# Performance work log

Measured on AMD Instinct MI355X. Metric: run time of the kernel, lower is better.

The kernel has to match this reference:

```python
import jax, jax.numpy as jnp
import numpy as np

NUM_EMBEDDINGS = 4096
EMBEDDING_DIM = 256


def setup_inputs() -> dict:
    key = jax.random.key(0)
    k1, k2 = jax.random.split(key)
    inputs = jax.random.normal(k1, (16, 4096, EMBEDDING_DIM), dtype=jnp.float32)
    embeddings = jax.random.normal(k2, (NUM_EMBEDDINGS, EMBEDDING_DIM), dtype=jnp.float32)
    return {"inputs": inputs, "embeddings": embeddings}


def reference(inputs, embeddings):
    input_shape = inputs.shape
    flat = inputs.reshape(-1, EMBEDDING_DIM)                     # [N, D]
    input_sq = jnp.sum(flat * flat, axis=1, keepdims=True)       # [N, 1]
    emb_sq = jnp.sum(embeddings * embeddings, axis=1)            # [K]
    distances = input_sq - 2.0 * (flat @ embeddings.T) + emb_sq  # [N, K]
    encoding_indices = jnp.argmin(distances, axis=1)             # [N]
    quantized = embeddings[encoding_indices].reshape(input_shape)
    encoding_indices = encoding_indices.reshape(input_shape[:-1])
    # use_commitment=False path: codebook loss only (quantized detached)
    loss = jnp.mean((jax.lax.stop_gradient(quantized) - inputs) ** 2)
    # straight-through estimator
    quantized_st = inputs + jax.lax.stop_gradient(quantized - inputs)
    return (quantized_st, loss, encoding_indices)
```

## Files before the change

### kernel.cpp

```cpp
#include <hip/hip_runtime.h>
#include <float.h>
#include <stdint.h>


#define DDIM 256
#define KCODES 4096
#define NROWS 65536
#define QSIZE 16777216
#define NSLOT 64
#define NLBLK 16384
#define GAP_THRESH 0.02f

#define O_FCOUNT 4097
#define O_FLAGS 4100
#define O_IDXF 69636
#define O_LPART 135172
#define O_EMBH 151556
#define O_EMBL 675844
#define O_AH 1200384
#define O_AL 9588992
#define WS_NEED_FLOATS 17977600ull

typedef short bf16x8 __attribute__((ext_vector_type(8)));
typedef float f32x4 __attribute__((ext_vector_type(4)));

__device__ __forceinline__ void gload_lds16(const void* g, void* l) {
    __builtin_amdgcn_global_load_lds(
        (const __attribute__((address_space(1))) void*)g,
        (__attribute__((address_space(3))) void*)l, 16, 0, 0);
}

__global__ __launch_bounds__(64) void esq_conv(const float* __restrict__ emb,
                                               float* __restrict__ ws,
                                               short* __restrict__ eh,
                                               short* __restrict__ el) {
    int c = blockIdx.x, l = threadIdx.x;
    const float4* e4 = (const float4*)(emb + (size_t)c * DDIM);
    float4 v = e4[l];
    float s = v.x * v.x + v.y * v.y + v.z * v.z + v.w * v.w;
    float f[4] = {v.x, v.y, v.z, v.w};
    uint32_t hu[4], lu[4];
#pragma unroll
    for (int k = 0; k < 4; ++k) {
        uint32_t u = __float_as_uint(f[k]);
        uint32_t h = u & 0xFFFF0000u;
        hu[k] = h;
        lu[k] = __float_as_uint(f[k] - __uint_as_float(h));
    }
    uint2 hv, lv;
    hv.x = __builtin_amdgcn_perm(hu[1], hu[0], 0x07060302u);
    hv.y = __builtin_amdgcn_perm(hu[3], hu[2], 0x07060302u);
    lv.x = __builtin_amdgcn_perm(lu[1], lu[0], 0x07060302u);
    lv.y = __builtin_amdgcn_perm(lu[3], lu[2], 0x07060302u);
    *(uint2*)&eh[(size_t)c * DDIM + l * 4] = hv;
    *(uint2*)&el[(size_t)c * DDIM + l * 4] = lv;
#pragma unroll
    for (int off = 32; off >= 1; off >>= 1) s += __shfl_down(s, off);
    if (l == 0) ws[c] = s;
    if (c == 0 && l == 0) ((int*)ws)[O_FCOUNT] = 0;
}

__device__ __forceinline__ void conv8(float4 a, float4 b,
                                      short* __restrict__ dh,
                                      short* __restrict__ dl) {
    float f[8] = {a.x, a.y, a.z, a.w, b.x, b.y, b.z, b.w};
    uint32_t hu[8], lu[8];
#pragma unroll
    for (int k = 0; k < 8; ++k) {
        uint32_t u = __float_as_uint(f[k]);
        uint32_t h = u & 0xFFFF0000u;
        hu[k] = h;
        lu[k] = __float_as_uint(f[k] - __uint_as_float(h));
    }
    uint4 hv, lv;
    hv.x = __builtin_amdgcn_perm(hu[1], hu[0], 0x07060302u);
    hv.y = __builtin_amdgcn_perm(hu[3], hu[2], 0x07060302u);
    hv.z = __builtin_amdgcn_perm(hu[5], hu[4], 0x07060302u);
    hv.w = __builtin_amdgcn_perm(hu[7], hu[6], 0x07060302u);
    lv.x = __builtin_amdgcn_perm(lu[1], lu[0], 0x07060302u);
    lv.y = __builtin_amdgcn_perm(lu[3], lu[2], 0x07060302u);
    lv.z = __builtin_amdgcn_perm(lu[5], lu[4], 0x07060302u);
    lv.w = __builtin_amdgcn_perm(lu[7], lu[6], 0x07060302u);
    *(uint4*)dh = hv;
    *(uint4*)dl = lv;
}

__device__ __forceinline__ void stage8(const float* __restrict__ p,
                                       short* __restrict__ dh,
                                       short* __restrict__ dl) {
    float4 a = *(const float4*)p;
    float4 b = *(const float4*)(p + 4);
    conv8(a, b, dh, dl);
}

__global__ __launch_bounds__(256) void inp_conv(const float* __restrict__ inp,
                                                short* __restrict__ ahg,
                                                short* __restrict__ alg) {
    size_t g = (size_t)blockIdx.x * 256 + threadIdx.x;
    const float* p = inp + g * 8;
    float4 a = *(const float4*)p;
    float4 b = *(const float4*)(p + 4);
    conv8(a, b, ahg + g * 8, alg + g * 8);
}

__global__ __launch_bounds__(512, 6) void vq_gemm(const short* __restrict__ ahg,
                                                  const short* __restrict__ alg,
                                                  const short* __restrict__ ehg,
                                                  const short* __restrict__ elg,
                                                  const float* __restrict__ esq,
                                                  float2* __restrict__ pmin2,
                                                  int* __restrict__ pidx) {
    __shared__ __align__(16) short Ah[128 * 32];
    __shared__ __align__(16) short Al[128 * 32];
    __shared__ __align__(16) short Bh[128 * 32];
    __shared__ __align__(16) short Bl[128 * 32];

    const int t = threadIdx.x;
    const int mi = blockIdx.x >> 5, ni = blockIdx.x & 31;
    const size_t row0 = (size_t)mi * 128;
    const int col0 = ni * 128;
    const int lane = t & 63, wave = t >> 6;
    const int wm = wave >> 1, wn = wave & 1;
    const int n15 = lane & 15, quad = lane >> 4;
    const int swz = (n15 >> 1) & 3;

    const int r0 = t >> 2, c0 = t & 3;
    const int p0 = c0 ^ ((r0 >> 1) & 3);
    const short* asrch = ahg + (size_t)(row0 + r0) * DDIM + p0 * 8;
    const short* asrcl = alg + (size_t)(row0 + r0) * DDIM + p0 * 8;
    const short* bsrch = ehg + (size_t)(col0 + r0) * DDIM + p0 * 8;
    const short* bsrcl = elg + (size_t)(col0 + r0) * DDIM + p0 * 8;
    const int d0 = t * 8;

    f32x4 acc[2][4];
#pragma unroll
    for (int i = 0; i < 2; ++i)
#pragma unroll
        for (int j = 0; j < 4; ++j) {
            acc[i][j][0] = 0.f; acc[i][j][1] = 0.f;
            acc[i][j][2] = 0.f; acc[i][j][3] = 0.f;
        }

#pragma unroll
    for (int ch = 0; ch < 8; ++ch) {
        __syncthreads();
        gload_lds16(asrch + ch * 32, &Ah[d0]);
        gload_lds16(asrcl + ch * 32, &Al[d0]);
        gload_lds16(bsrch + ch * 32, &Bh[d0]);
        gload_lds16(bsrcl + ch * 32, &Bl[d0]);
        __syncthreads();

        bf16x8 ah[2], al[2];
#pragma unroll
        for (int i = 0; i < 2; ++i) {
            int off = (wm * 32 + i * 16 + n15) * 32 + ((quad ^ swz) * 8);
            ah[i] = *(const bf16x8*)&Ah[off];
            al[i] = *(const bf16x8*)&Al[off];
        }
#pragma unroll
        for (int j = 0; j < 4; ++j) {
            int boff = (wn * 64 + j * 16 + n15) * 32 + ((quad ^ swz) * 8);
            bf16x8 bh = *(const bf16x8*)&Bh[boff];
            bf16x8 bl = *(const bf16x8*)&Bl[boff];
#pragma unroll
            for (int i = 0; i < 2; ++i) {
                acc[i][j] = __builtin_amdgcn_mfma_f32_16x16x32_bf16(ah[i], bh, acc[i][j], 0, 0, 0);
                acc[i][j] = __builtin_amdgcn_mfma_f32_16x16x32_bf16(ah[i], bl, acc[i][j], 0, 0, 0);
                acc[i][j] = __builtin_amdgcn_mfma_f32_16x16x32_bf16(al[i], bh, acc[i][j], 0, 0, 0);
            }
        }
    }

    float esqv[4];
#pragma unroll
    for (int j = 0; j < 4; ++j) esqv[j] = esq[col0 + wn * 64 + j * 16 + n15];

#pragma unroll
    for (int i = 0; i < 2; ++i) {
#pragma unroll
        for (int reg = 0; reg < 4; ++reg) {
            float m1 = FLT_MAX, m2 = FLT_MAX;
            int bi = 0;
#pragma unroll
            for (int j = 0; j < 4; ++j) {
                float d = esqv[j] - 2.0f * acc[i][j][reg];
                int code = col0 + wn * 64 + j * 16 + n15;
                if (d < m1) { m2 = m1; m1 = d; bi = code; }
                else if (d < m2) { m2 = d; }
            }
#pragma unroll
            for (int off = 1; off < 16; off <<= 1) {
                float om1 = __shfl_xor(m1, off);
                float om2 = __shfl_xor(m2, off);
                int obi = __shfl_xor(bi, off);
                bool take = (om1 < m1) || (om1 == m1 && obi < bi);
                if (take) { m2 = fminf(m1, om2); m1 = om1; bi = obi; }
                else      { m2 = fminf(om1, m2); }
            }
            if (n15 == 0) {
                int rg = (int)row0 + wm * 32 + i * 16 + quad * 4 + reg;
                int slot = ni * 2 + wn;
                pmin2[(size_t)slot * NROWS + rg] = make_float2(m1, m2);
                pidx[(size_t)slot * NROWS + rg] = bi;
            }
        }
    }
}

__global__ __launch_bounds__(256, 2) void vq_gemm_fb(const float* __restrict__ inp,
                                                     const short* __restrict__ ehg,
                                                     const short* __restrict__ elg,
                                                     const float* __restrict__ esq,
                                                     float2* __restrict__ pmin2,
                                                     int* __restrict__ pidx) {
    __shared__ __align__(16) short Ah[128 * 32];
    __shared__ __align__(16) short Al[128 * 32];
    __shared__ __align__(16) short Bh[128 * 32];
    __shared__ __align__(16) short Bl[128 * 32];

    const int t = threadIdx.x;
    const int mi = blockIdx.x >> 5, ni = blockIdx.x & 31;
    const size_t row0 = (size_t)mi * 128;
    const int col0 = ni * 128;
    const int lane = t & 63, wave = t >> 6;
    const int wm = wave >> 1, wn = wave & 1;
    const int n15 = lane & 15, quad = lane >> 4;
    const int swz = (n15 >> 1) & 3;

    const int ar0 = t >> 2, ac0 = t & 3;
    const int ap0 = ac0 ^ ((ar0 >> 1) & 3);
    const int ar1 = (t + 256) >> 2, ac1 = ac0;
    const int ap1 = ac1 ^ ((ar1 >> 1) & 3);
    const float* asrc0 = inp + (row0 + ar0) * DDIM + ac0 * 8;
    const float* asrc1 = inp + (row0 + ar1) * DDIM + ac1 * 8;
    short* adst0h = &Ah[ar0 * 32 + ap0 * 8];
    short* adst0l = &Al[ar0 * 32 + ap0 * 8];
    short* adst1h = &Ah[ar1 * 32 + ap1 * 8];
    short* adst1l = &Al[ar1 * 32 + ap1 * 8];
    const int br0 = ar0, bp0 = ac0, bk0 = bp0 ^ ((br0 >> 1) & 3);
    const int br1 = ar1, bp1 = ac1, bk1 = bp1 ^ ((br1 >> 1) & 3);
    const short* bsrc0h = ehg + (size_t)(col0 + br0) * DDIM + bk0 * 8;
    const short* bsrc0l = elg + (size_t)(col0 + br0) * DDIM + bk0 * 8;
    const short* bsrc1h = ehg + (size_t)(col0 + br1) * DDIM + bk1 * 8;
    const short* bsrc1l = elg + (size_t)(col0 + br1) * DDIM + bk1 * 8;

    f32x4 acc[4][4];
#pragma unroll
    for (int i = 0; i < 4; ++i)
#pragma unroll
        for (int j = 0; j < 4; ++j) {
            acc[i][j][0] = 0.f; acc[i][j][1] = 0.f;
            acc[i][j][2] = 0.f; acc[i][j][3] = 0.f;
        }

#pragma unroll
    for (int ch = 0; ch < 8; ++ch) {
        __syncthreads();
        gload_lds16(bsrc0h + ch * 32, &Bh[t * 8]);
        gload_lds16(bsrc0l + ch * 32, &Bl[t * 8]);
        gload_lds16(bsrc1h + ch * 32, &Bh[(t + 256) * 8]);
        gload_lds16(bsrc1l + ch * 32, &Bl[(t + 256) * 8]);
        stage8(asrc0 + ch * 32, adst0h, adst0l);
        stage8(asrc1 + ch * 32, adst1h, adst1l);
        __syncthreads();

        bf16x8 ah[4], al[4];
#pragma unroll
        for (int i = 0; i < 4; ++i) {
            int off = (wm * 64 + i * 16 + n15) * 32 + ((quad ^ swz) * 8);
            ah[i] = *(const bf16x8*)&Ah[off];
            al[i] = *(const bf16x8*)&Al[off];
        }
#pragma unroll
        for (int j = 0; j < 4; ++j) {
            int boff = (wn * 64 + j * 16 + n15) * 32 + ((quad ^ swz) * 8);
            bf16x8 bh = *(const bf16x8*)&Bh[boff];
            bf16x8 bl = *(const bf16x8*)&Bl[boff];
#pragma unroll
            for (int i = 0; i < 4; ++i) {
                acc[i][j] = __builtin_amdgcn_mfma_f32_16x16x32_bf16(ah[i], bh, acc[i][j], 0, 0, 0);
                acc[i][j] = __builtin_amdgcn_mfma_f32_16x16x32_bf16(ah[i], bl, acc[i][j], 0, 0, 0);
                acc[i][j] = __builtin_amdgcn_mfma_f32_16x16x32_bf16(al[i], bh, acc[i][j], 0, 0, 0);
            }
        }
    }

    float esqv[4];
#pragma unroll
    for (int j = 0; j < 4; ++j) esqv[j] = esq[col0 + wn * 64 + j * 16 + n15];

#pragma unroll
    for (int i = 0; i < 4; ++i) {
#pragma unroll
        for (int reg = 0; reg < 4; ++reg) {
            float m1 = FLT_MAX, m2 = FLT_MAX;
            int bi = 0;
#pragma unroll
            for (int j = 0; j < 4; ++j) {
                float d = esqv[j] - 2.0f * acc[i][j][reg];
                int code = col0 + wn * 64 + j * 16 + n15;
                if (d < m1) { m2 = m1; m1 = d; bi = code; }
                else if (d < m2) { m2 = d; }
            }
#pragma unroll
            for (int off = 1; off < 16; off <<= 1) {
                float om1 = __shfl_xor(m1, off);
                float om2 = __shfl_xor(m2, off);
                int obi = __shfl_xor(bi, off);
                bool take = (om1 < m1) || (om1 == m1 && obi < bi);
                if (take) { m2 = fminf(m1, om2); m1 = om1; bi = obi; }
                else      { m2 = fminf(om1, m2); }
            }
            if (n15 == 0) {
                int rg = (int)row0 + wm * 64 + i * 16 + quad * 4 + reg;
                int slot = ni * 2 + wn;
                pmin2[(size_t)slot * NROWS + rg] = make_float2(m1, m2);
                pidx[(size_t)slot * NROWS + rg] = bi;
            }
        }
    }
}

__global__ __launch_bounds__(256) void vq_reduce(const float2* __restrict__ pmin2,
                                                 const int* __restrict__ pidx,
                                                 int* __restrict__ idx_final,
                                                 int* __restrict__ flags,
                                                 int* __restrict__ fcount) {
    int row = blockIdx.x * 256 + threadIdx.x;
    float m1 = FLT_MAX, m2 = FLT_MAX;
    int bi = 0;
    for (int nb = 0; nb < NSLOT; ++nb) {
        float2 p = pmin2[(size_t)nb * NROWS + row];
        int pi = pidx[(size_t)nb * NROWS + row];
        if (p.x < m1) { m2 = fminf(m1, p.y); m1 = p.x; bi = pi; }
        else          { m2 = fminf(m2, p.x); }
    }
    idx_final[row] = bi;
    if (m2 - m1 < GAP_THRESH) {
        int s = atomicAdd(fcount, 1);
        flags[s] = row;
    }
}

__global__ __launch_bounds__(256) void vq_recheck(const float* __restrict__ inp,
                                                  const float* __restrict__ emb,
                                                  const float* __restrict__ esq,
                                                  const int* __restrict__ flags,
                                                  const int* __restrict__ fcount,
                                                  int* __restrict__ idx_final) {
    __shared__ float4 xs[64];
    __shared__ float sv[4];
    __shared__ int si[4];
    const int t = threadIdx.x;
    const int cnt = *fcount;
    for (int f = blockIdx.x; f < cnt; f += gridDim.x) {
        int row = flags[f];
        __syncthreads();
        if (t < 64) xs[t] = ((const float4*)inp)[(size_t)row * 64 + t];
        __syncthreads();
        float m1 = FLT_MAX;
        int bi = 0x7FFFFFFF;
        for (int cc = 0; cc < 16; ++cc) {
            int c = cc * 256 + t;
            const float4* e4 = (const float4*)emb + (size_t)c * 64;
            float dot = 0.f;
            for (int d4 = 0; d4 < 64; ++d4) {
                float4 e = e4[d4];
                float4 x = xs[d4];
                dot += e.x * x.x; dot += e.y * x.y;
                dot += e.z * x.z; dot += e.w * x.w;
            }
            float d = esq[c] - 2.0f * dot;
            if (d < m1 || (d == m1 && c < bi)) { m1 = d; bi = c; }
        }
#pragma unroll
        for (int off = 1; off < 64; off <<= 1) {
            float om = __shfl_xor(m1, off);
            int ob = __shfl_xor(bi, off);
            if (om < m1 || (om == m1 && ob < bi)) { m1 = om; bi = ob; }
        }
        if ((t & 63) == 0) { sv[t >> 6] = m1; si[t >> 6] = bi; }
        __syncthreads();
        if (t == 0) {
            for (int w = 1; w < 4; ++w)
                if (sv[w] < m1 || (sv[w] == m1 && si[w] < bi)) { m1 = sv[w]; bi = si[w]; }
            idx_final[row] = bi;
        }
    }
}

__global__ __launch_bounds__(256) void vq_gather(const float* __restrict__ inp,
                                                 const float* __restrict__ emb,
                                                 const int* __restrict__ idx_final,
                                                 float* __restrict__ out,
                                                 float* __restrict__ loss_part) {
    __shared__ float wsum[4];
    size_t gid = (size_t)blockIdx.x * 256 + threadIdx.x;
    int row = (int)(gid >> 6), c4 = (int)(gid & 63);
    int k = idx_final[row];
    float4 e = ((const float4*)emb)[(size_t)k * 64 + c4];
    float4 x = ((const float4*)inp)[gid];
    ((float4*)out)[gid] = e;
    float dx = e.x - x.x, dy = e.y - x.y, dz = e.z - x.z, dw = e.w - x.w;
    float ls = dx * dx + dy * dy + dz * dz + dw * dw;
#pragma unroll
    for (int off = 32; off >= 1; off >>= 1) ls += __shfl_down(ls, off);
    if ((threadIdx.x & 63) == 0) wsum[threadIdx.x >> 6] = ls;
    if (c4 == 0) out[(size_t)QSIZE + 1 + row] = (float)k;
    __syncthreads();
    if (threadIdx.x == 0)
        loss_part[blockIdx.x] = wsum[0] + wsum[1] + wsum[2] + wsum[3];
}

__global__ __launch_bounds__(256) void loss_kernel(const float* __restrict__ loss_part,
                                                   float* __restrict__ out) {
    __shared__ float sw[4];
    int t = threadIdx.x;
    float s = 0.0f;
    for (int i = t; i < NLBLK; i += 256) s += loss_part[i];
#pragma unroll
    for (int off = 32; off >= 1; off >>= 1) s += __shfl_down(s, off);
    if ((t & 63) == 0) sw[t >> 6] = s;
    __syncthreads();
    if (t == 0)
        out[QSIZE] = (sw[0] + sw[1] + sw[2] + sw[3]) * (1.0f / 16777216.0f);
}

extern "C" void kernel_launch(void* const* d_in, const int* in_sizes, int n_in,
                              void* d_out, int out_size, void* d_ws, size_t ws_size,
                              hipStream_t stream) {
    const float* inp = (const float*)d_in[0];
    const float* emb = (const float*)d_in[1];
    float* out = (float*)d_out;
    float* ws = (float*)d_ws;

    float* esq = ws;
    int* fcount = (int*)ws + O_FCOUNT;
    int* flags = (int*)ws + O_FLAGS;
    int* idx_final = (int*)ws + O_IDXF;
    float* loss_part = ws + O_LPART;
    short* eh = (short*)(ws + O_EMBH);
    short* el = (short*)(ws + O_EMBL);

    float2* pmin2 = (float2*)out;
    int* pidx = (int*)out + 8388608;

    hipLaunchKernelGGL(esq_conv, dim3(KCODES), dim3(64), 0, stream, emb, ws, eh, el);

    if (ws_size >= WS_NEED_FLOATS * 4ull) {
        short* ah = (short*)(ws + O_AH);
        short* al = (short*)(ws + O_AL);
        hipLaunchKernelGGL(inp_conv, dim3(8192), dim3(256), 0, stream, inp, ah, al);
        hipLaunchKernelGGL(vq_gemm, dim3((NROWS / 128) * 32), dim3(512), 0, stream,
                           ah, al, eh, el, esq, pmin2, pidx);
    } else {
        hipLaunchKernelGGL(vq_gemm_fb, dim3((NROWS / 128) * 32), dim3(256), 0, stream,
                           inp, eh, el, esq, pmin2, pidx);
    }

    hipLaunchKernelGGL(vq_reduce, dim3(NROWS / 256), dim3(256), 0, stream,
                       pmin2, pidx, idx_final, flags, fcount);
    hipLaunchKernelGGL(vq_recheck, dim3(1024), dim3(256), 0, stream,
                       inp, emb, esq, flags, fcount, idx_final);
    hipLaunchKernelGGL(vq_gather, dim3(NLBLK), dim3(256), 0, stream,
                       inp, emb, idx_final, out, loss_part);
    hipLaunchKernelGGL(loss_kernel, dim3(1), dim3(256), 0, stream, loss_part, out);
}
```

Baseline: 771.7 us.

## Split exact recheck of ambiguous rows across codebook chunks with atomicMin keys

The exact fp32 recheck of rows whose top-2 distance gap is small is split into 16 work items per flagged row, each covering 256 codes. Each item reduces an order-preserving packed (distance, index) 64-bit key and combines it with an atomicMin into a per-row key slot. A small unpack kernel then writes the winning indices. This spreads the recheck over many more blocks so it is not serialized on one block per row. The cost is extra workspace, one extra launch and 64-bit atomics, and the workspace-size threshold for taking the fast path rises.

```diff
diff --git a/kernel.cpp b/kernel.cpp
--- a/kernel.cpp
+++ b/kernel.cpp
@@ -19,7 +19,8 @@
 #define O_EMBL 675844
 #define O_AH 1200384
 #define O_AL 9588992
-#define WS_NEED_FLOATS 17977600ull
+#define O_KEYS 17977600
+#define WS_NEED_FLOATS 18108672ull
 
 typedef short bf16x8 __attribute__((ext_vector_type(8)));
 typedef float f32x4 __attribute__((ext_vector_type(4)));
@@ -325,7 +326,8 @@
                                                  const int* __restrict__ pidx,
                                                  int* __restrict__ idx_final,
                                                  int* __restrict__ flags,
-                                                 int* __restrict__ fcount) {
+                                                 int* __restrict__ fcount,
+                                                 unsigned long long* __restrict__ keys) {
     int row = blockIdx.x * 256 + threadIdx.x;
     float m1 = FLT_MAX, m2 = FLT_MAX;
     int bi = 0;
@@ -339,7 +341,62 @@
     if (m2 - m1 < GAP_THRESH) {
         int s = atomicAdd(fcount, 1);
         flags[s] = row;
-    }
+        if (keys) keys[s] = 0xFFFFFFFFFFFFFFFFull;
+    }
+}
+
+__global__ __launch_bounds__(256) void vq_recheck2(const float* __restrict__ inp,
+                                                   const float* __restrict__ emb,
+                                                   const float* __restrict__ esq,
+                                                   const int* __restrict__ flags,
+                                                   const int* __restrict__ fcount,
+                                                   unsigned long long* __restrict__ keys) {
+    __shared__ float4 xs[64];
+    __shared__ unsigned long long wbest[4];
+    const int t = threadIdx.x;
+    const int total = (*fcount) * 16;
+    for (int wi = blockIdx.x; wi < total; wi += gridDim.x) {
+        const int fi = wi >> 4, cb = wi & 15;
+        const int row = flags[fi];
+        __syncthreads();
+        if (t < 64) xs[t] = ((const float4*)inp)[(size_t)row * 64 + t];
+        __syncthreads();
+        const int c = cb * 256 + t;
+        const float4* e4 = (const float4*)emb + (size_t)c * 64;
+        float dot = 0.f;
+        for (int d4 = 0; d4 < 64; ++d4) {
+            float4 e = e4[d4];
+            float4 x = xs[d4];
+            dot += e.x * x.x; dot += e.y * x.y;
+            dot += e.z * x.z; dot += e.w * x.w;
+        }
+        float d = esq[c] - 2.0f * dot;
+        unsigned u = __float_as_uint(d);
+        unsigned skey = (u & 0x80000000u) ? ~u : (u | 0x80000000u);
+        unsigned long long k = ((unsigned long long)skey << 32) | (unsigned)c;
+#pragma unroll
+        for (int off = 1; off < 64; off <<= 1) {
+            unsigned long long o = __shfl_xor(k, off);
+            if (o < k) k = o;
+        }
+        if ((t & 63) == 0) wbest[t >> 6] = k;
+        __syncthreads();
+        if (t == 0) {
+            unsigned long long b = wbest[0];
+            if (wbest[1] < b) b = wbest[1];
+            if (wbest[2] < b) b = wbest[2];
+            if (wbest[3] < b) b = wbest[3];
+            atomicMin(&keys[fi], b);
+        }
+    }
+}
+
+__global__ __launch_bounds__(256) void vq_unpack(const int* __restrict__ flags,
+                                                 const int* __restrict__ fcount,
+                                                 const unsigned long long* __restrict__ keys,
+                                                 int* __restrict__ idx_final) {
+    int i = blockIdx.x * 256 + threadIdx.x;
+    if (i < *fcount) idx_final[flags[i]] = (int)(keys[i] & 0xFFFFFFFFull);
 }
 
 __global__ __launch_bounds__(256) void vq_recheck(const float* __restrict__ inp,
@@ -450,18 +507,26 @@
     if (ws_size >= WS_NEED_FLOATS * 4ull) {
         short* ah = (short*)(ws + O_AH);
         short* al = (short*)(ws + O_AL);
+        unsigned long long* keys = (unsigned long long*)(ws + O_KEYS);
         hipLaunchKernelGGL(inp_conv, dim3(8192), dim3(256), 0, stream, inp, ah, al);
         hipLaunchKernelGGL(vq_gemm, dim3((NROWS / 128) * 32), dim3(512), 0, stream,
                            ah, al, eh, el, esq, pmin2, pidx);
+        hipLaunchKernelGGL(vq_reduce, dim3(NROWS / 256), dim3(256), 0, stream,
+                           pmin2, pidx, idx_final, flags, fcount, keys);
+        hipLaunchKernelGGL(vq_recheck2, dim3(8192), dim3(256), 0, stream,
+                           inp, emb, esq, flags, fcount, keys);
+        hipLaunchKernelGGL(vq_unpack, dim3(NROWS / 256), dim3(256), 0, stream,
+                           flags, fcount, keys, idx_final);
     } else {
         hipLaunchKernelGGL(vq_gemm_fb, dim3((NROWS / 128) * 32), dim3(256), 0, stream,
                            inp, eh, el, esq, pmin2, pidx);
-    }
-
-    hipLaunchKernelGGL(vq_reduce, dim3(NROWS / 256), dim3(256), 0, stream,
-                       pmin2, pidx, idx_final, flags, fcount);
-    hipLaunchKernelGGL(vq_recheck, dim3(1024), dim3(256), 0, stream,
-                       inp, emb, esq, flags, fcount, idx_final);
+        hipLaunchKernelGGL(vq_reduce, dim3(NROWS / 256), dim3(256), 0, stream,
+                           pmin2, pidx, idx_final, flags, fcount,
+                           (unsigned long long*)nullptr);
+        hipLaunchKernelGGL(vq_recheck, dim3(256), dim3(256), 0, stream,
+                           inp, emb, esq, flags, fcount, idx_final);
+    }
+
     hipLaunchKernelGGL(vq_gather, dim3(NLBLK), dim3(256), 0, stream,
                        inp, emb, idx_final, out, loss_part);
     hipLaunchKernelGGL(loss_kernel, dim3(1), dim3(256), 0, stream, loss_part, out);
```

Result: faster. 736.2 us (-4.6%).
